# Kernel tuning notes

Measured on AMD Instinct MI355X. Metric: run time of the kernel, lower is better.

Reference implementation:

```python
import jax, jax.numpy as jnp
import numpy as np
from jax import lax

B, C_VIS, C_GRAPH, C_OUT, H, W, K = 8, 256, 256, 256, 96, 96, 3


def conv2d(x, w, b):
    # x: [B,Cin,H,W], w: [Cout,Cin,K,K], SAME padding (pad = K//2)
    y = lax.conv_general_dilated(x, w, window_strides=(1, 1), padding='SAME',
                                 dimension_numbers=('NCHW', 'OIHW', 'NCHW'))
    return y + b[None, :, None, None]


def setup_inputs() -> dict:
    key = jax.random.key(0)
    ks = jax.random.split(key, 12)
    scale_v = 1.0 / np.sqrt(C_VIS * K * K)
    scale_g = 1.0 / np.sqrt(C_GRAPH * K * K)
    scale_o = 1.0 / np.sqrt(C_OUT * K * K)
    return {
        'feats': jax.random.normal(ks[0], (B, C_VIS, H, W), jnp.float32),
        'graph_feature': jax.random.normal(ks[1], (B, C_GRAPH, H, W), jnp.float32),
        'wq': jax.random.normal(ks[2], (C_OUT, C_GRAPH, K, K), jnp.float32) * scale_g,
        'bq': jax.random.normal(ks[3], (C_OUT,), jnp.float32) * 0.01,
        'wk': jax.random.normal(ks[4], (C_OUT, C_VIS, K, K), jnp.float32) * scale_v,
        'bk': jax.random.normal(ks[5], (C_OUT,), jnp.float32) * 0.01,
        'wv': jax.random.normal(ks[6], (C_OUT, C_VIS, K, K), jnp.float32) * scale_v,
        'bv': jax.random.normal(ks[7], (C_OUT,), jnp.float32) * 0.01,
        'wo': jax.random.normal(ks[8], (C_OUT, C_OUT, K, K), jnp.float32) * scale_o,
        'bo': jax.random.normal(ks[9], (C_OUT,), jnp.float32) * 0.01,
    }


def reference(feats, graph_feature, wq, bq, wk, bk, wv, bv, wo, bo):
    q = conv2d(graph_feature, wq, bq)  # [B,C,H,W]
    k = conv2d(feats, wk, bk)          # [B,C,H,W]
    v = conv2d(feats, wv, bv)          # [B,C,H,W]
    # attention over rows: attn[b,c,i,j] = sum_w q[b,c,i,w] * k[b,c,j,w]
    scale = 1.0 / jnp.sqrt(jnp.asarray(k.shape[-1], q.dtype))
    attn = jnp.einsum('bchw,bcgw->bchg', q, k) * scale  # [B,C,H,H]
    attn = jax.nn.softmax(attn, axis=-1)
    fused = jnp.einsum('bchg,bcgw->bchw', attn, v)      # [B,C,H,W]
    return conv2d(fused, wo, bo)
```

## Files before the change

### kernel.cpp

```cpp
#include <hip/hip_runtime.h>
#include <hip/hip_bf16.h>

constexpr int BATCH = 8;
constexpr int CH    = 256;
constexpr int H     = 96;
constexpr int W     = 96;
constexpr int HW    = H * W;
constexpr long PLANE_ELEMS = (long)BATCH * CH * HW;
constexpr int PAD   = 98;

typedef short  bf16x8_t __attribute__((ext_vector_type(8)));
typedef float  f32x4_t  __attribute__((ext_vector_type(4)));

__device__ inline uint pk2_bf16(float a, float b) {
  ushort lo = __bfloat16_as_ushort(__float2bfloat16(a));
  ushort hi = __bfloat16_as_ushort(__float2bfloat16(b));
  return (uint)lo | ((uint)hi << 16);
}

#define WAITVM(N) asm volatile("s_waitcnt vmcnt(" #N ")" ::: "memory")

__device__ __forceinline__ void gl_lds16(const ushort* g, ushort* l) {
  __builtin_amdgcn_global_load_lds(
      (const __attribute__((address_space(1))) void*)g,
      (__attribute__((address_space(3))) void*)l, 16, 0, 0);
}

__global__ __launch_bounds__(256) void border_zero(
    ushort* __restrict__ p0, ushort* __restrict__ p1)
{
  const int u = blockIdx.x * 256 + threadIdx.x;
  if (u >= 12416) return;
  const int b = blockIdx.y;
  ushort* p = blockIdx.z ? p1 : p0;
  int y, x, cu;
  if (u < 6272)      { y = (u < 3136) ? 0 : 97; int r = u % 3136; x = r >> 5; cu = r & 31; }
  else               { int r = u - 6272; x = (r < 3072) ? 0 : 97; int r2 = r % 3072; y = 1 + (r2 >> 5); cu = r2 & 31; }
  int4 z = make_int4(0, 0, 0, 0);
  *(int4*)&p[(((long)b * PAD + y) * PAD + x) * 256 + cu * 8] = z;
}

__global__ __launch_bounds__(256) void nchw_f32_to_nhwc_bf16_2(
    const float* __restrict__ in0, const float* __restrict__ in1,
    ushort* __restrict__ out0, ushort* __restrict__ out1)
{
  __shared__ float t[32][33];
  const int tid = threadIdx.x;
  const int p0 = blockIdx.x * 32;
  const int c0 = blockIdx.y * 32;
  const int ts = blockIdx.z >> 3;
  const int b  = blockIdx.z & 7;
  const float* in = ts ? in1 : in0;
  ushort* out     = ts ? out1 : out0;
  const int tp = tid & 31, tc8 = tid >> 5;
#pragma unroll
  for (int i = 0; i < 4; ++i) {
    int c = tc8 + i * 8;
    t[c][tp] = in[((long)(b * 256 + c0 + c)) * HW + p0 + tp];
  }
  __syncthreads();
  const int wc = tid & 31, wp8 = tid >> 5;
#pragma unroll
  for (int i = 0; i < 4; ++i) {
    int p = p0 + wp8 + i * 8;
    int y = p / 96, x = p % 96;
    out[(((long)b * PAD + y + 1) * PAD + x + 1) * 256 + c0 + wc] =
        __bfloat16_as_ushort(__float2bfloat16(t[wc][wp8 + i * 8]));
  }
}

__global__ __launch_bounds__(256) void nchw_bf16_to_nhwc_bf16(
    const ushort* __restrict__ in, ushort* __restrict__ out)
{
  __shared__ ushort t[32][34];
  const int tid = threadIdx.x;
  const int p0 = blockIdx.x * 32;
  const int c0 = blockIdx.y * 32;
  const int b  = blockIdx.z;
  const int tp = tid & 31, tc8 = tid >> 5;
#pragma unroll
  for (int i = 0; i < 4; ++i) {
    int c = tc8 + i * 8;
    t[c][tp] = in[((long)(b * 256 + c0 + c)) * HW + p0 + tp];
  }
  __syncthreads();
  const int wc = tid & 31, wp8 = tid >> 5;
#pragma unroll
  for (int i = 0; i < 4; ++i) {
    int p = p0 + wp8 + i * 8;
    int y = p / 96, x = p % 96;
    out[(((long)b * PAD + y + 1) * PAD + x + 1) * 256 + c0 + wc] = t[wc][wp8 + i * 8];
  }
}

__global__ __launch_bounds__(256) void w_prep4(
    const float* __restrict__ s0, const float* __restrict__ s1,
    const float* __restrict__ s2, const float* __restrict__ s3,
    ushort* __restrict__ d0, ushort* __restrict__ d1,
    ushort* __restrict__ d2, ushort* __restrict__ d3)
{
  const int t = blockIdx.x / 2304;
  const int idx = (blockIdx.x % 2304) * 256 + threadIdx.x;
  const float* s = (t == 0) ? s0 : (t == 1) ? s1 : (t == 2) ? s2 : s3;
  ushort* d      = (t == 0) ? d0 : (t == 1) ? d1 : (t == 2) ? d2 : d3;
  int ci  = idx & 255;
  int co  = (idx >> 8) & 255;
  int tap = idx >> 16;
  d[idx] = __bfloat16_as_ushort(__float2bfloat16(s[(co * 256 + ci) * 9 + tap]));
}

template <int NT, typename OutT>
__global__ __launch_bounds__(256, 2) void conv3x3_mfma(
    const ushort* pin0, const ushort* pin1,
    const ushort* w0, const ushort* w1, const ushort* w2,
    const float* bias0, const float* bias1, const float* bias2,
    OutT* o0, OutT* o1, OutT* o2)
{
  const int tid  = threadIdx.x;
  const int lane = tid & 63;
  const int wv   = tid >> 6;
  const int wm   = wv & 1;
  const int wn   = wv >> 1;
  const int l15  = lane & 15;
  const int lg   = lane >> 4;

  const int nwg = NT * 768;
  const int cpx = nwg >> 3;
  const int swz = ((int)blockIdx.x & 7) * cpx + ((int)blockIdx.x >> 3);
  const int t    = swz / 768;
  const int rest = swz % 768;
  const ushort* pin = (t == 2) ? pin1 : pin0;
  const ushort* wt  = (t == 0) ? w0 : (t == 1) ? w1 : w2;
  const float* bias = (t == 0) ? bias0 : (t == 1) ? bias1 : bias2;
  OutT* out         = (t == 0) ? o0 : (t == 1) ? o1 : o2;

  const int cox = rest & 1;
  const int yb  = (rest >> 1) % 48;
  const int b   = (rest >> 1) / 48;
  const int co0 = cox * 128;
  const int y0  = yb * 2;

  __shared__ ushort sIn[2][1568 * 8];
  __shared__ ushort sA [3][512 * 8];

  f32x4_t acc[4][6];
#pragma unroll
  for (int m = 0; m < 4; ++m)
#pragma unroll
    for (int n = 0; n < 6; ++n)
      acc[m][n] = (f32x4_t){0.f, 0.f, 0.f, 0.f};

  const int aoff = (lg ^ ((l15 + (l15 >> 2)) & 3)) << 4;

  auto issueA = [&](int cc, int tap, int slot) {
    if (cc >= 8) return;
    const int ci0 = cc * 32;
#pragma unroll
    for (int r = 0; r < 2; ++r) {
      int L  = r * 256 + wv * 64 + lane;
      int co = L >> 2;
      int u  = (L & 3) ^ ((co + (co >> 2)) & 3);
      const ushort* src = wt + ((tap * 256 + co0 + co) << 8) + ci0 + u * 8;
      ushort* dst = (ushort*)((char*)&sA[slot][0] + (r * 256 + wv * 64) * 16);
      gl_lds16(src, dst);
    }
  };

  auto issueIN = [&](int cc) {
    const int ci0 = cc * 32;
    const int ubase = wv * 392;
#pragma unroll
    for (int it = 0; it < 7; ++it) {
      int lo = it * 64 + lane;
      if (lo < 392) {
        int u  = ubase + lo;
        int q  = u >> 2;
        int g  = u & 3;
        int xx = q % 98, rr = q / 98;
        int ug = g ^ ((xx + (xx >> 2)) & 3);
        const ushort* src = pin + (((long)(b * PAD + y0 + rr)) * PAD + xx) * 256 + ci0 + ug * 8;
        ushort* dst = (ushort*)((char*)&sIn[cc & 1][0] + (long)u * 16);
        gl_lds16(src, dst);
      }
    }
  };

  auto dotap = [&](int DY, int DX, int bi, int slot) {
    bf16x8_t a[4], bb[6];
    const char* Ab = (const char*)&sA[slot][0];
#pragma unroll
    for (int m = 0; m < 4; ++m)
      a[m] = *(const bf16x8_t*)(Ab + ((wm * 64 + m * 16 + l15) << 6) + aoff);
    const char* Bb = (const char*)&sIn[bi][0];
    const int s    = l15 + DX;
    const int boff = (lg ^ ((s + (s >> 2)) & 3)) << 4;
    const int rr   = wn + DY;
#pragma unroll
    for (int n = 0; n < 6; ++n)
      bb[n] = *(const bf16x8_t*)(Bb + ((rr * 98 + n * 16 + s) << 6) + boff);
    __builtin_amdgcn_s_setprio(1);
#pragma unroll
    for (int m = 0; m < 4; ++m)
#pragma unroll
      for (int n = 0; n < 6; ++n)
        acc[m][n] = __builtin_amdgcn_mfma_f32_16x16x32_bf16(
            a[m], bb[n], acc[m][n], 0, 0, 0);
    __builtin_amdgcn_s_setprio(0);
  };

#define CPHASE(TAP, VMN, EXTRA)                                            \
  WAITVM(VMN);                                                             \
  __builtin_amdgcn_s_barrier();                                            \
  __builtin_amdgcn_sched_barrier(0);                                       \
  issueA(c + (TAP + 2) / 9, (TAP + 2) % 9, (TAP + 2) % 3);                 \
  EXTRA                                                                    \
  dotap(TAP / 3, TAP % 3, c & 1, TAP % 3);

  issueA(0, 0, 0);
  issueA(0, 1, 1);
  issueIN(0);
  WAITVM(0);
  __builtin_amdgcn_s_barrier();
  __builtin_amdgcn_sched_barrier(0);

#pragma unroll 1
  for (int c = 0; c < 7; ++c) {
    CPHASE(0, 2, )
    CPHASE(1, 2, )
    CPHASE(2, 2, issueIN(c + 1);)
    CPHASE(3, 9, )
    CPHASE(4, 9, )
    CPHASE(5, 2, )
    CPHASE(6, 2, )
    CPHASE(7, 2, )
    CPHASE(8, 2, )
  }
  {
    const int c = 7;
    CPHASE(0, 2, )
    CPHASE(1, 2, )
    CPHASE(2, 2, )
    CPHASE(3, 2, )
    CPHASE(4, 2, )
    CPHASE(5, 2, )
    CPHASE(6, 2, )
    CPHASE(7, 2, )
    CPHASE(8, 0, )
  }
#undef CPHASE

  const int y = y0 + wn;
  if constexpr (sizeof(OutT) == 2) {
    char* sE = (char*)&sIn[0][0];
    __syncthreads();
#pragma unroll
    for (int h = 0; h < 2; ++h) {
      if (wm == h) {
#pragma unroll
        for (int m = 0; m < 4; ++m)
#pragma unroll
          for (int r = 0; r < 4; ++r) {
            const int col = m * 16 + lg * 4 + r;
            const float bv = bias[co0 + h * 64 + col];
#pragma unroll
            for (int n = 0; n < 6; ++n) {
              *(ushort*)(sE + col * 400 + (wn * 96 + n * 16 + l15) * 2) =
                  __bfloat16_as_ushort(__float2bfloat16(acc[m][n][r] + bv));
            }
          }
      }
      __syncthreads();
#pragma unroll
      for (int it = 0; it < 7; ++it) {
        int u = it * 256 + tid;
        if (u < 1600) {
          int co = u / 25, ru = u % 25;
          if (ru < 24) {
            int4 v = *(const int4*)(sE + co * 400 + ru * 16);
            int e0 = ru * 8;
            int yy = y0 + (e0 >= 96);
            int x  = e0 - (e0 >= 96 ? 96 : 0);
            *(int4*)&out[(((long)(b * 256 + co0 + h * 64 + co)) * 96 + yy) * 96 + x] = v;
          }
        }
      }
      __syncthreads();
    }
  } else {
#pragma unroll
    for (int m = 0; m < 4; ++m) {
      const int cobase = co0 + wm * 64 + m * 16 + lg * 4;
#pragma unroll
      for (int r = 0; r < 4; ++r) {
        const int co = cobase + r;
        const float bv = bias[co];
#pragma unroll
        for (int n = 0; n < 6; ++n) {
          out[((long)(b * 256 + co) * 96 + y) * 96 + n * 16 + l15] =
              acc[m][n][r] + bv;
        }
      }
    }
  }
}

constexpr int APITCH = 104;

__global__ __launch_bounds__(384, 3) void attn_mfma(
    const ushort* __restrict__ q,
    const ushort* __restrict__ k,
    const ushort* __restrict__ v,
    ushort* __restrict__ outf)
{
  __shared__ ushort sK [96 * APITCH];
  __shared__ ushort sVt[96 * APITCH];
  __shared__ ushort sP [6 * 16 * APITCH];

  const int tid  = threadIdx.x;
  const int lane = tid & 63;
  const int wv   = tid >> 6;
  const int l15  = lane & 15;
  const int lg   = lane >> 4;
  const long plane = (long)blockIdx.x * HW;

  for (int u = tid; u < 1152; u += 384) {
    int j = u / 12, c8 = u % 12;
    *(int4*)&sK[j * APITCH + c8 * 8] = *(const int4*)&k[plane + j * 96 + c8 * 8];
  }
  for (int u = tid; u < 1152; u += 384) {
    int j = u % 96, c8 = u / 96;
    ushort tmp[8];
    *(int4*)tmp = *(const int4*)&v[plane + j * 96 + c8 * 8];
#pragma unroll
    for (int e = 0; e < 8; ++e)
      sVt[(c8 * 8 + e) * APITCH + j] = tmp[e];
  }
  __syncthreads();

  const int i0 = wv * 16;

  bf16x8_t qf[3];
#pragma unroll
  for (int ks = 0; ks < 3; ++ks)
    qf[ks] = *(const bf16x8_t*)&q[plane + (i0 + l15) * 96 + ks * 32 + lg * 8];

  f32x4_t s[6];
#pragma unroll
  for (int jt = 0; jt < 6; ++jt) s[jt] = (f32x4_t){0.f, 0.f, 0.f, 0.f};
#pragma unroll
  for (int jt = 0; jt < 6; ++jt)
#pragma unroll
    for (int ks = 0; ks < 3; ++ks) {
      bf16x8_t kf = *(const bf16x8_t*)&sK[(jt * 16 + l15) * APITCH + ks * 32 + lg * 8];
      s[jt] = __builtin_amdgcn_mfma_f32_16x16x32_bf16(kf, qf[ks], s[jt], 0, 0, 0);
    }

  const float sc = 0.10206207261596575f;
  float m = -3.0e38f;
#pragma unroll
  for (int jt = 0; jt < 6; ++jt)
#pragma unroll
    for (int r = 0; r < 4; ++r) m = fmaxf(m, s[jt][r]);
  m = fmaxf(m, __shfl_xor(m, 16));
  m = fmaxf(m, __shfl_xor(m, 32));

  float p[6][4];
  float sum = 0.f;
#pragma unroll
  for (int jt = 0; jt < 6; ++jt)
#pragma unroll
    for (int r = 0; r < 4; ++r) {
      float e = __expf((s[jt][r] - m) * sc);
      p[jt][r] = e;
      sum += e;
    }
  sum += __shfl_xor(sum, 16);
  sum += __shfl_xor(sum, 32);
  const float inv = 1.f / sum;

  ushort* myP = &sP[wv * 16 * APITCH];
#pragma unroll
  for (int jt = 0; jt < 6; ++jt) {
    *(uint*)&myP[l15 * APITCH + jt * 16 + lg * 4] =
        pk2_bf16(p[jt][0] * inv, p[jt][1] * inv);
    *(uint*)&myP[l15 * APITCH + jt * 16 + lg * 4 + 2] =
        pk2_bf16(p[jt][2] * inv, p[jt][3] * inv);
  }

  bf16x8_t pf[3];
#pragma unroll
  for (int ks = 0; ks < 3; ++ks)
    pf[ks] = *(const bf16x8_t*)&myP[l15 * APITCH + ks * 32 + lg * 8];

  f32x4_t o[6];
#pragma unroll
  for (int wt = 0; wt < 6; ++wt) o[wt] = (f32x4_t){0.f, 0.f, 0.f, 0.f};
#pragma unroll
  for (int wt = 0; wt < 6; ++wt)
#pragma unroll
    for (int ks = 0; ks < 3; ++ks) {
      bf16x8_t vf = *(const bf16x8_t*)&sVt[(wt * 16 + l15) * APITCH + ks * 32 + lg * 8];
      o[wt] = __builtin_amdgcn_mfma_f32_16x16x32_bf16(pf[ks], vf, o[wt], 0, 0, 0);
    }

#pragma unroll
  for (int wt = 0; wt < 6; ++wt)
#pragma unroll
    for (int r = 0; r < 4; ++r) {
      int i = i0 + lg * 4 + r;
      outf[plane + i * 96 + wt * 16 + l15] =
          __bfloat16_as_ushort(__float2bfloat16(o[wt][r]));
    }
}

extern "C" void kernel_launch(void* const* d_in, const int* in_sizes, int n_in,
                              void* d_out, int out_size, void* d_ws, size_t ws_size,
                              hipStream_t stream) {
  (void)in_sizes; (void)n_in; (void)out_size; (void)ws_size;

  const float* feats = (const float*)d_in[0];
  const float* graph = (const float*)d_in[1];
  const float* wq    = (const float*)d_in[2];
  const float* bq    = (const float*)d_in[3];
  const float* wk    = (const float*)d_in[4];
  const float* bk    = (const float*)d_in[5];
  const float* wv    = (const float*)d_in[6];
  const float* bv    = (const float*)d_in[7];
  const float* wo    = (const float*)d_in[8];
  const float* bo    = (const float*)d_in[9];
  float* out = (float*)d_out;

  char* ws = (char*)d_ws;
  const long planeB   = PLANE_ELEMS * 2;
  const long pinElems = (long)BATCH * PAD * PAD * 256;
  ushort* qb   = (ushort*)ws;
  ushort* kb   = (ushort*)(ws + planeB);
  ushort* vb   = (ushort*)(ws + 2 * planeB);
  ushort* pinF = (ushort*)(ws + 3 * planeB);
  ushort* pinG = pinF + pinElems;
  ushort* wtq  = pinG + pinElems;
  ushort* wtk  = wtq + 9 * 256 * 256;
  ushort* wtv  = wtk + 9 * 256 * 256;
  ushort* wto  = wtv + 9 * 256 * 256;

  dim3 tgrid2(HW / 32, CH / 32, 2 * BATCH);
  dim3 tgrid (HW / 32, CH / 32, BATCH);
  dim3 agrid (BATCH * CH);
  dim3 bgrid (49, BATCH, 2);

  border_zero<<<bgrid, 256, 0, stream>>>(pinF, pinG);

  w_prep4<<<4 * 2304, 256, 0, stream>>>(wq, wk, wv, wo, wtq, wtk, wtv, wto);

  nchw_f32_to_nhwc_bf16_2<<<tgrid2, 256, 0, stream>>>(feats, graph, pinF, pinG);

  conv3x3_mfma<3, ushort><<<3 * 768, 256, 0, stream>>>(
      pinF, pinG, wtk, wtv, wtq, bk, bv, bq, kb, vb, qb);

  attn_mfma<<<agrid, 384, 0, stream>>>(qb, kb, vb, qb);

  nchw_bf16_to_nhwc_bf16<<<tgrid, 256, 0, stream>>>(qb, pinF);

  conv3x3_mfma<1, float><<<768, 256, 0, stream>>>(
      pinF, pinF, wto, wto, wto, bo, bo, bo, out, out, out);
}
```

Measured before the change: 488.1 us.

## Load conv weights directly to registers in MFMA layout, drop LDS weight staging

```diff
diff --git a/kernel.cpp b/kernel.cpp
--- a/kernel.cpp
+++ b/kernel.cpp
@@ -103,9 +103,14 @@
   const int idx = (blockIdx.x % 2304) * 256 + threadIdx.x;
   const float* s = (t == 0) ? s0 : (t == 1) ? s1 : (t == 2) ? s2 : s3;
   ushort* d      = (t == 0) ? d0 : (t == 1) ? d1 : (t == 2) ? d2 : d3;
-  int ci  = idx & 255;
-  int co  = (idx >> 8) & 255;
-  int tap = idx >> 16;
+  const int e   = idx & 7;
+  const int lg  = (idx >> 3) & 3;
+  const int l15 = (idx >> 5) & 15;
+  const int q   = (idx >> 9) & 15;
+  const int cc  = (idx >> 13) & 7;
+  const int tap = idx >> 16;
+  const int co  = q * 16 + l15;
+  const int ci  = cc * 32 + lg * 8 + e;
   d[idx] = __bfloat16_as_ushort(__float2bfloat16(s[(co * 256 + ci) * 9 + tap]));
 }
 
@@ -139,9 +144,10 @@
   const int b   = (rest >> 1) / 48;
   const int co0 = cox * 128;
   const int y0  = yb * 2;
+  const int coq = cox * 8 + wm * 4;
+  const int alo = (l15 * 4 + lg) << 3;
 
   __shared__ ushort sIn[2][1568 * 8];
-  __shared__ ushort sA [3][512 * 8];
 
   f32x4_t acc[4][6];
 #pragma unroll
@@ -149,22 +155,6 @@
 #pragma unroll
     for (int n = 0; n < 6; ++n)
       acc[m][n] = (f32x4_t){0.f, 0.f, 0.f, 0.f};
-
-  const int aoff = (lg ^ ((l15 + (l15 >> 2)) & 3)) << 4;
-
-  auto issueA = [&](int cc, int tap, int slot) {
-    if (cc >= 8) return;
-    const int ci0 = cc * 32;
-#pragma unroll
-    for (int r = 0; r < 2; ++r) {
-      int L  = r * 256 + wv * 64 + lane;
-      int co = L >> 2;
-      int u  = (L & 3) ^ ((co + (co >> 2)) & 3);
-      const ushort* src = wt + ((tap * 256 + co0 + co) << 8) + ci0 + u * 8;
-      ushort* dst = (ushort*)((char*)&sA[slot][0] + (r * 256 + wv * 64) * 16);
-      gl_lds16(src, dst);
-    }
-  };
 
   auto issueIN = [&](int cc) {
     const int ci0 = cc * 32;
@@ -185,12 +175,22 @@
     }
   };
 
-  auto dotap = [&](int DY, int DX, int bi, int slot) {
-    bf16x8_t a[4], bb[6];
-    const char* Ab = (const char*)&sA[slot][0];
-#pragma unroll
-    for (int m = 0; m < 4; ++m)
-      a[m] = *(const bf16x8_t*)(Ab + ((wm * 64 + m * 16 + l15) << 6) + aoff);
+  auto glda = [&](int tap, int cc, int m) -> bf16x8_t {
+    return *(const bf16x8_t*)&wt[(((tap * 8 + cc) * 16 + coq + m) << 9) + alo];
+  };
+
+  bf16x8_t a0[4], a1[4], a2[4];
+
+#define ISSUE_A(CC, TAP, AR)                \
+  if ((CC) < 8) {                           \
+    AR[0] = glda((TAP), (CC), 0);           \
+    AR[1] = glda((TAP), (CC), 1);           \
+    AR[2] = glda((TAP), (CC), 2);           \
+    AR[3] = glda((TAP), (CC), 3);           \
+  }
+
+  auto dotap = [&](int DY, int DX, int bi, const bf16x8_t* a) {
+    bf16x8_t bb[6];
     const char* Bb = (const char*)&sIn[bi][0];
     const int s    = l15 + DX;
     const int boff = (lg ^ ((s + (s >> 2)) & 3)) << 4;
@@ -208,51 +208,38 @@
     __builtin_amdgcn_s_setprio(0);
   };
 
-#define CPHASE(TAP, VMN, EXTRA)                                            \
-  WAITVM(VMN);                                                             \
-  __builtin_amdgcn_s_barrier();                                            \
-  __builtin_amdgcn_sched_barrier(0);                                       \
-  issueA(c + (TAP + 2) / 9, (TAP + 2) % 9, (TAP + 2) % 3);                 \
-  EXTRA                                                                    \
-  dotap(TAP / 3, TAP % 3, c & 1, TAP % 3);
-
-  issueA(0, 0, 0);
-  issueA(0, 1, 1);
   issueIN(0);
-  WAITVM(0);
+  __builtin_amdgcn_sched_barrier(0);
+  ISSUE_A(0, 0, a0);
+  ISSUE_A(0, 1, a1);
+  __builtin_amdgcn_sched_barrier(0);
+  WAITVM(8);
   __builtin_amdgcn_s_barrier();
   __builtin_amdgcn_sched_barrier(0);
 
 #pragma unroll 1
-  for (int c = 0; c < 7; ++c) {
-    CPHASE(0, 2, )
-    CPHASE(1, 2, )
-    CPHASE(2, 2, issueIN(c + 1);)
-    CPHASE(3, 9, )
-    CPHASE(4, 9, )
-    CPHASE(5, 2, )
-    CPHASE(6, 2, )
-    CPHASE(7, 2, )
-    CPHASE(8, 2, )
-  }
-  {
-    const int c = 7;
-    CPHASE(0, 2, )
-    CPHASE(1, 2, )
-    CPHASE(2, 2, )
-    CPHASE(3, 2, )
-    CPHASE(4, 2, )
-    CPHASE(5, 2, )
-    CPHASE(6, 2, )
-    CPHASE(7, 2, )
-    CPHASE(8, 0, )
-  }
-#undef CPHASE
-
-  const int y = y0 + wn;
+  for (int c = 0; c < 8; ++c) {
+    const int bi = c & 1;
+    ISSUE_A(c, 2, a2)  dotap(0, 0, bi, a0);
+    ISSUE_A(c, 3, a0)  dotap(0, 1, bi, a1);
+    ISSUE_A(c, 4, a1)  dotap(0, 2, bi, a2);
+    ISSUE_A(c, 5, a2)  dotap(1, 0, bi, a0);
+    ISSUE_A(c, 6, a0)  dotap(1, 1, bi, a1);
+    ISSUE_A(c, 7, a1)  dotap(1, 2, bi, a2);
+    ISSUE_A(c, 8, a2)  dotap(2, 0, bi, a0);
+    if (c < 7) issueIN(c + 1);
+    __builtin_amdgcn_sched_barrier(0);
+    ISSUE_A(c + 1, 0, a0)  dotap(2, 1, bi, a1);
+    ISSUE_A(c + 1, 1, a1)  dotap(2, 2, bi, a2);
+    __builtin_amdgcn_sched_barrier(0);
+    if (c < 7) { WAITVM(8); } else { WAITVM(0); }
+    __builtin_amdgcn_s_barrier();
+    __builtin_amdgcn_sched_barrier(0);
+  }
+#undef ISSUE_A
+
   if constexpr (sizeof(OutT) == 2) {
     char* sE = (char*)&sIn[0][0];
-    __syncthreads();
 #pragma unroll
     for (int h = 0; h < 2; ++h) {
       if (wm == h) {
@@ -287,19 +274,35 @@
       __syncthreads();
     }
   } else {
-#pragma unroll
-    for (int m = 0; m < 4; ++m) {
-      const int cobase = co0 + wm * 64 + m * 16 + lg * 4;
-#pragma unroll
-      for (int r = 0; r < 4; ++r) {
-        const int co = cobase + r;
-        const float bv = bias[co];
-#pragma unroll
-        for (int n = 0; n < 6; ++n) {
-          out[((long)(b * 256 + co) * 96 + y) * 96 + n * 16 + l15] =
-              acc[m][n][r] + bv;
-        }
+    char* sE = (char*)&sIn[0][0];
+#pragma unroll
+    for (int h = 0; h < 2; ++h) {
+      if (wm == h) {
+#pragma unroll
+        for (int m = 0; m < 4; ++m)
+#pragma unroll
+          for (int r = 0; r < 4; ++r) {
+            const int col = m * 16 + lg * 4 + r;
+            const float bv = bias[co0 + h * 64 + col];
+#pragma unroll
+            for (int n = 0; n < 6; ++n) {
+              *(float*)(sE + (col * 196 + wn * 96 + n * 16 + l15) * 4) =
+                  acc[m][n][r] + bv;
+            }
+          }
       }
+      __syncthreads();
+#pragma unroll
+      for (int it = 0; it < 12; ++it) {
+        int u = it * 256 + tid;
+        int co = u / 48, ru = u % 48;
+        int4 v = *(const int4*)(sE + (co * 196 + ru * 4) * 4);
+        int e0 = ru * 4;
+        int yy = y0 + (e0 >= 96);
+        int x  = e0 - (e0 >= 96 ? 96 : 0);
+        *(int4*)&out[(((long)(b * 256 + co0 + h * 64 + co)) * 96 + yy) * 96 + x] = v;
+      }
+      __syncthreads();
     }
   }
 }
```

Measured after the change: 397.7 us. -18.5%, faster.
